# Kernel optimization log

Hardware: AMD Instinct MI355X
Metric: run time of the kernel (lower is better)

## Reference

```python
import jax, jax.numpy as jnp
import numpy as np

NUM_EMBEDDINGS = 1024
EMBEDDING_DIM = 256
BETA = 0.25


def setup_inputs() -> dict:
    key = jax.random.key(0)
    kz, ke = jax.random.split(key)
    z = jax.random.normal(kz, (32, EMBEDDING_DIM, 32, 32), dtype=jnp.float32)
    # codebook initialized uniform(-1/K, 1/K) as in the torch module
    emb = jax.random.uniform(ke, (NUM_EMBEDDINGS, EMBEDDING_DIM), dtype=jnp.float32,
                             minval=-1.0 / NUM_EMBEDDINGS, maxval=1.0 / NUM_EMBEDDINGS)
    return {"z": z, "emb": emb}


def reference(z, emb):
    B, C, H, W = z.shape
    # [B, C, H, W] -> [B*H*W, C]
    z_flat = jnp.transpose(z, (0, 2, 3, 1)).reshape(-1, C)
    # squared L2 distances to every codebook entry: [N, K]
    distances = (jnp.sum(z_flat ** 2, axis=1, keepdims=True)
                 + jnp.sum(emb ** 2, axis=1)
                 - 2.0 * jnp.matmul(z_flat, emb.T))
    indices = jnp.argmin(distances, axis=1).reshape(B, H, W)  # int32 [B, H, W]
    # gather codebook vectors, back to [B, C, H, W]
    z_q = jnp.transpose(emb[indices], (0, 3, 1, 2))
    sg = jax.lax.stop_gradient
    loss = (BETA * jnp.mean((sg(z_q) - z) ** 2)
            + jnp.mean((z_q - sg(z)) ** 2))
    # straight-through estimator
    z_q_st = z + sg(z_q - z)
    return z_q_st, indices, loss
```

## Files before the change

### kernel.cpp

```cpp
#include <hip/hip_runtime.h>

#define CDIM 256
#define HW 1024
#define NROWS 32768
#define KCODES 1024
#define ZQ_ELEMS 8388608
#define IDX_OFF ZQ_ELEMS
#define LOSS_OFF (ZQ_ELEMS + NROWS)
#define FLT_BIG 3.402823466e+38f
#define ZT_OFF 5513232ull

typedef _Float16 f16;
typedef _Float16 f16x8 __attribute__((ext_vector_type(8)));
typedef float f32x4 __attribute__((ext_vector_type(4)));
typedef float f32x16 __attribute__((ext_vector_type(16)));

__device__ __forceinline__ void glds16(const void* g, void* l) {
    __builtin_amdgcn_global_load_lds(
        (const __attribute__((address_space(1))) unsigned int*)g,
        (__attribute__((address_space(3))) unsigned int*)l,
        16, 0, 0);
}

__device__ __forceinline__ unsigned int pack_f16x2(f16 a, f16 b) {
    unsigned short ua = *(unsigned short*)&a, ub = *(unsigned short*)&b;
    return (unsigned int)ua | ((unsigned int)ub << 16);
}

__device__ __forceinline__ float np_sumsq_256(const float* __restrict__ a) {
    float half[2];
#pragma unroll
    for (int h = 0; h < 2; ++h) {
        const float* p = a + h * 128;
        float r[8];
#pragma unroll
        for (int j = 0; j < 8; ++j) r[j] = __fmul_rn(p[j], p[j]);
#pragma unroll
        for (int i = 8; i < 128; i += 8) {
#pragma unroll
            for (int j = 0; j < 8; ++j)
                r[j] = __fadd_rn(r[j], __fmul_rn(p[i + j], p[i + j]));
        }
        float ta = __fadd_rn(__fadd_rn(r[0], r[1]), __fadd_rn(r[2], r[3]));
        float tb = __fadd_rn(__fadd_rn(r[4], r[5]), __fadd_rn(r[6], r[7]));
        half[h] = __fadd_rn(ta, tb);
    }
    return __fadd_rn(half[0], half[1]);
}

__device__ __forceinline__ bool lex_lt(float s1, int k1, float s2, int k2) {
    return (s1 < s2) || (s1 == s2 && k1 < k2);
}

__device__ __forceinline__ void top2_merge(float& a1, int& ka1, float& a2, int& ka2,
                                           float b1, int kb1, float b2, int kb2) {
    if (lex_lt(b1, kb1, a1, ka1)) {
        float t1 = a1; int tk1 = ka1;
        a1 = b1; ka1 = kb1;
        if (lex_lt(b2, kb2, t1, tk1)) { a2 = b2; ka2 = kb2; }
        else                          { a2 = t1; ka2 = tk1; }
    } else {
        if (lex_lt(b1, kb1, a2, ka2)) { a2 = b1; ka2 = kb1; }
    }
}

__global__ void __launch_bounds__(256)
prep_kernel(const float* __restrict__ z, const float* __restrict__ emb,
            f16* __restrict__ A, float* __restrict__ z2,
            float* __restrict__ e2, f16* __restrict__ e16,
            float* __restrict__ z_t) {
    const int t = threadIdx.x;
    if (blockIdx.x >= 1024) {
        const int gid = (blockIdx.x - 1024) * 256 + t;
        const int k = gid >> 5, seg = gid & 31;
        const float* src = emb + (size_t)k * CDIM + seg * 8;
        float4 v0 = *(const float4*)src;
        float4 v1 = *(const float4*)(src + 4);
        float s[8] = { v0.x, v0.y, v0.z, v0.w, v1.x, v1.y, v1.z, v1.w };
        f16 h[8], l[8];
#pragma unroll
        for (int j = 0; j < 8; ++j) {
            float sv = s[j] * 1024.0f;
            h[j] = (f16)sv;
            float r = __fsub_rn(sv, (float)h[j]);
            l[j] = (f16)r;
        }
        uint4 hv, lv;
        hv.x = pack_f16x2(h[0], h[1]); hv.y = pack_f16x2(h[2], h[3]);
        hv.z = pack_f16x2(h[4], h[5]); hv.w = pack_f16x2(h[6], h[7]);
        lv.x = pack_f16x2(l[0], l[1]); lv.y = pack_f16x2(l[2], l[3]);
        lv.z = pack_f16x2(l[4], l[5]); lv.w = pack_f16x2(l[6], l[7]);
        *(uint4*)(e16 + (size_t)k * 512 + seg * 8) = hv;
        *(uint4*)(e16 + (size_t)k * 512 + 256 + seg * 8) = lv;
        if (seg == 0) e2[k] = np_sumsq_256(emb + (size_t)k * CDIM);
        return;
    }
    __shared__ __align__(16) float z_lds[32 * 260];
    const int n0 = blockIdx.x * 32;
    const int b = n0 >> 10, hw0 = n0 & 1023;
    const float* zbase = z + (size_t)b * (CDIM * HW) + hw0;
#pragma unroll
    for (int p = 0; p < 8; ++p) {
        int id = p * 256 + t;
        int c = id >> 3;
        int m4 = id & 7;
        float4 v = *(const float4*)(zbase + (size_t)c * HW + m4 * 4);
        z_lds[(m4 * 4 + 0) * 260 + c] = v.x;
        z_lds[(m4 * 4 + 1) * 260 + c] = v.y;
        z_lds[(m4 * 4 + 2) * 260 + c] = v.z;
        z_lds[(m4 * 4 + 3) * 260 + c] = v.w;
    }
    __syncthreads();
    if (t < 32) z2[n0 + t] = np_sumsq_256(&z_lds[t * 260]);

    if (z_t) {
#pragma unroll
        for (int p = 0; p < 8; ++p) {
            int id = p * 256 + t;
            int m = id >> 6;
            int c4 = (id & 63) * 4;
            float4 v = { z_lds[m * 260 + c4],     z_lds[m * 260 + c4 + 1],
                         z_lds[m * 260 + c4 + 2], z_lds[m * 260 + c4 + 3] };
            *(float4*)&z_t[(size_t)(n0 + m) * CDIM + c4] = v;
        }
    }

    const int lane = t & 63, wave = t >> 6;
    const int half = lane >> 5;
    const int seg = lane & 31;
#pragma unroll
    for (int rr = 0; rr < 8; ++rr) {
        const int m = wave * 8 + rr;
        const float* zr = &z_lds[m * 260 + seg * 8];
        f16 o[8];
#pragma unroll
        for (int j = 0; j < 8; ++j) {
            float sv = zr[j] * 16.0f;
            f16 hh = (f16)sv;
            if (half) {
                float r = __fsub_rn(sv, (float)hh);
                o[j] = (f16)r;
            } else {
                o[j] = hh;
            }
        }
        uint4 ov;
        ov.x = pack_f16x2(o[0], o[1]); ov.y = pack_f16x2(o[2], o[3]);
        ov.z = pack_f16x2(o[4], o[5]); ov.w = pack_f16x2(o[6], o[7]);
        *(uint4*)(A + (size_t)(n0 + m) * 512 + half * 256 + seg * 8) = ov;
    }
}

__global__ void __launch_bounds__(256, 3)
gemm_argmin_kernel(const f16* __restrict__ A, const f16* __restrict__ B,
                   const float* __restrict__ z2, const float* __restrict__ e2,
                   float4* __restrict__ tile_red) {
    __shared__ __align__(16) f16 c1_lds[2][128 * 32];
    __shared__ __align__(16) f16 c2_lds[2][128 * 32];
    __shared__ __align__(16) f16 z_lds[2][128 * 32];
    __shared__ __align__(16) float4 red_lds[2 * 128];
    __shared__ float e2_lds[128];

    const int t = threadIdx.x;
    const int lane = t & 63, wave = t >> 6;
    const int Ntile = blockIdx.x & 255;
    const int Mtile = blockIdx.x >> 8;
    const int wc = (wave & 1) * 64;
    const int wz = (wave >> 1) * 64;
    const int c31 = lane & 31, hhalf = lane >> 5;
    const int gsw = (c31 >> 1) & 3;

    if (t < 128) e2_lds[t] = e2[Mtile * 128 + t];

    const int s0 = 2 * wave, s1 = s0 + 1;
    const char* Cbase = (const char*)(B + (size_t)Mtile * 128 * 512);
    const char* Zbase = (const char*)(A + (size_t)Ntile * 128 * 512);
    const int lrow = lane >> 2;
    const int lsw = ((lane & 3) ^ ((lrow >> 1) & 3)) * 16;
    const char* cg0 = Cbase + (size_t)(s0 * 16 + lrow) * 1024 + lsw;
    const char* cg1 = Cbase + (size_t)(s1 * 16 + lrow) * 1024 + lsw;
    const char* zg0 = Zbase + (size_t)(s0 * 16 + lrow) * 1024 + lsw;
    const char* zg1 = Zbase + (size_t)(s1 * 16 + lrow) * 1024 + lsw;

    int crow32[2], zrow32[2], g8[2];
#pragma unroll
    for (int i = 0; i < 2; ++i) crow32[i] = (wc + i * 32 + c31) * 32;
#pragma unroll
    for (int j = 0; j < 2; ++j) zrow32[j] = (wz + j * 32 + c31) * 32;
#pragma unroll
    for (int ks = 0; ks < 2; ++ks) g8[ks] = ((2 * ks + hhalf) ^ gsw) * 8;

    f32x16 acc[2][2] = {};

    glds16(cg0,       &c1_lds[0][s0 * 512]);
    glds16(cg1,       &c1_lds[0][s1 * 512]);
    glds16(cg0 + 512, &c2_lds[0][s0 * 512]);
    glds16(cg1 + 512, &c2_lds[0][s1 * 512]);
    glds16(zg0,       &z_lds[0][s0 * 512]);
    glds16(zg1,       &z_lds[0][s1 * 512]);
    __syncthreads();

    for (int kk = 0; kk < 16; ++kk) {
        const int buf = kk & 1;
        if (kk < 15) {
            const int nb = buf ^ 1;
            const int ko = (kk + 1) * 64;
            const int ko2 = (ko + 512) & 1023;
            glds16(cg0 + ko,  &c1_lds[nb][s0 * 512]);
            glds16(cg1 + ko,  &c1_lds[nb][s1 * 512]);
            glds16(cg0 + ko2, &c2_lds[nb][s0 * 512]);
            glds16(cg1 + ko2, &c2_lds[nb][s1 * 512]);
            glds16(zg0 + ko,  &z_lds[nb][s0 * 512]);
            glds16(zg1 + ko,  &z_lds[nb][s1 * 512]);
        }

#pragma unroll
        for (int ks = 0; ks < 2; ++ks) {
            f16x8 zf[2], cf1[2], cf2[2];
#pragma unroll
            for (int j = 0; j < 2; ++j)
                zf[j] = *(const f16x8*)&z_lds[buf][zrow32[j] + g8[ks]];
#pragma unroll
            for (int i = 0; i < 2; ++i) {
                cf1[i] = *(const f16x8*)&c1_lds[buf][crow32[i] + g8[ks]];
                cf2[i] = *(const f16x8*)&c2_lds[buf][crow32[i] + g8[ks]];
            }
#pragma unroll
            for (int i = 0; i < 2; ++i)
#pragma unroll
                for (int j = 0; j < 2; ++j) {
                    acc[i][j] = __builtin_amdgcn_mfma_f32_32x32x16_f16(cf1[i], zf[j], acc[i][j], 0, 0, 0);
                    acc[i][j] = __builtin_amdgcn_mfma_f32_32x32x16_f16(cf2[i], zf[j], acc[i][j], 0, 0, 0);
                }
        }
        __syncthreads();
    }

#pragma unroll
    for (int j = 0; j < 2; ++j) {
        const float z2v = z2[Ntile * 128 + wz + j * 32 + c31];
        float s1 = FLT_BIG, s2 = FLT_BIG;
        int k1 = KCODES, k2 = KCODES;
#pragma unroll
        for (int i = 0; i < 2; ++i) {
            const int cbase = wc + i * 32 + 4 * hhalf;
#pragma unroll
            for (int r = 0; r < 16; ++r) {
                const int clocal = cbase + (r & 3) + 8 * (r >> 2);
                const float e2r = e2_lds[clocal];
                const float d = __fsub_rn(__fadd_rn(z2v, e2r),
                                          __fmul_rn(acc[i][j][r], 1.220703125e-4f));
                const int kc = Mtile * 128 + clocal;
                if (lex_lt(d, kc, s1, k1)) { s2 = s1; k2 = k1; s1 = d; k1 = kc; }
                else if (lex_lt(d, kc, s2, k2)) { s2 = d; k2 = kc; }
            }
        }
        float b1 = __shfl_xor(s1, 32); int kb1 = __shfl_xor(k1, 32);
        float b2 = __shfl_xor(s2, 32); int kb2 = __shfl_xor(k2, 32);
        top2_merge(s1, k1, s2, k2, b1, kb1, b2, kb2);
        if (hhalf == 0) {
            float4 st;
            st.x = s1; st.y = __int_as_float(k1);
            st.z = s2; st.w = __int_as_float(k2);
            red_lds[(wave & 1) * 128 + wz + j * 32 + c31] = st;
        }
    }
    __syncthreads();
    if (t < 128) {
        float4 a = red_lds[t];
        float4 b = red_lds[128 + t];
        float a1 = a.x, a2 = a.z; int ka1 = __float_as_int(a.y), ka2 = __float_as_int(a.w);
        top2_merge(a1, ka1, a2, ka2, b.x, __float_as_int(b.y), b.z, __float_as_int(b.w));
        float4 o;
        o.x = a1; o.y = __int_as_float(ka1); o.z = a2; o.w = __int_as_float(ka2);
        tile_red[(size_t)(Ntile * 128 + t) * 8 + Mtile] = o;
    }
}

__global__ void __launch_bounds__(256)
rescore_kernel(const float* __restrict__ z, const float* __restrict__ emb,
               const float* __restrict__ z2, const float* __restrict__ e2,
               const float4* __restrict__ tile_red, const float* __restrict__ z_t,
               float* __restrict__ out_idx_f, int* __restrict__ ws_idx) {
    const int gid = blockIdx.x * 256 + threadIdx.x;
    const int n = gid >> 2, q = gid & 3;

    float s[4]; int k[4];
    const float4 v0 = tile_red[(size_t)n * 8 + q * 2];
    const float4 v1 = tile_red[(size_t)n * 8 + q * 2 + 1];
    s[0] = v0.x; k[0] = __float_as_int(v0.y);
    s[1] = v0.z; k[1] = __float_as_int(v0.w);
    s[2] = v1.x; k[2] = __float_as_int(v1.y);
    s[3] = v1.z; k[3] = __float_as_int(v1.w);

    float s1 = FLT_BIG; int k1 = KCODES;
#pragma unroll
    for (int i = 0; i < 4; ++i)
        if (lex_lt(s[i], k[i], s1, k1)) { s1 = s[i]; k1 = k[i]; }
#pragma unroll
    for (int m = 1; m <= 2; m <<= 1) {
        float bs = __shfl_xor(s1, m); int bk2 = __shfl_xor(k1, m);
        if (lex_lt(bs, bk2, s1, k1)) { s1 = bs; k1 = bk2; }
    }
    const float thr = s1 + 1.0e-4f;
    int cnt = 0;
#pragma unroll
    for (int i = 0; i < 4; ++i) cnt += (s[i] <= thr) ? 1 : 0;
    cnt += __shfl_xor(cnt, 1);
    cnt += __shfl_xor(cnt, 2);

    int bk = k1;
    if (cnt > 1) {
        int kk[4];
#pragma unroll
        for (int i = 0; i < 4; ++i) kk[i] = (s[i] <= thr) ? k[i] : k1;
        float accs[4] = { 0.f, 0.f, 0.f, 0.f };
        if (z_t) {
            const float* zr = z_t + (size_t)n * CDIM;
            for (int c0 = 0; c0 < 256; c0 += 4) {
                const float4 zv = *(const float4*)&zr[c0];
#pragma unroll
                for (int j = 0; j < 4; ++j) {
                    float4 ev = *(const float4*)&emb[(size_t)kk[j] * CDIM + c0];
                    accs[j] = fmaf(zv.x, ev.x, accs[j]);
                    accs[j] = fmaf(zv.y, ev.y, accs[j]);
                    accs[j] = fmaf(zv.z, ev.z, accs[j]);
                    accs[j] = fmaf(zv.w, ev.w, accs[j]);
                }
            }
        } else {
            const float* zb = z + (size_t)(n >> 10) * (CDIM * HW) + (n & 1023);
            for (int c0 = 0; c0 < 256; c0 += 4) {
                float zc0 = zb[(size_t)(c0 + 0) * HW];
                float zc1 = zb[(size_t)(c0 + 1) * HW];
                float zc2 = zb[(size_t)(c0 + 2) * HW];
                float zc3 = zb[(size_t)(c0 + 3) * HW];
#pragma unroll
                for (int j = 0; j < 4; ++j) {
                    float4 ev = *(const float4*)&emb[(size_t)kk[j] * CDIM + c0];
                    accs[j] = fmaf(zc0, ev.x, accs[j]);
                    accs[j] = fmaf(zc1, ev.y, accs[j]);
                    accs[j] = fmaf(zc2, ev.z, accs[j]);
                    accs[j] = fmaf(zc3, ev.w, accs[j]);
                }
            }
        }
        float bd = FLT_BIG; bk = KCODES;
        const float z2n = z2[n];
#pragma unroll
        for (int j = 0; j < 4; ++j) {
            float d = __fsub_rn(__fadd_rn(z2n, e2[kk[j]]), accs[j] + accs[j]);
            if (lex_lt(d, kk[j], bd, bk)) { bd = d; bk = kk[j]; }
        }
#pragma unroll
        for (int m = 1; m <= 2; m <<= 1) {
            float bs = __shfl_xor(bd, m); int bb = __shfl_xor(bk, m);
            if (lex_lt(bs, bb, bd, bk)) { bd = bs; bk = bb; }
        }
    }
    if (q == 0) {
        out_idx_f[n] = (float)bk;
        ws_idx[n] = bk;
    }
}

__global__ void __launch_bounds__(256)
gather_kernel(const float* __restrict__ z, const float* __restrict__ emb,
              const int* __restrict__ ws_idx, float* __restrict__ out_zq,
              float* __restrict__ partials) {
    const int t = threadIdx.x;
    const int b = blockIdx.x >> 5;
    const int cg = blockIdx.x & 31;
    const int hw4 = t * 4;

    const int4 iv = *(const int4*)&ws_idx[b * HW + hw4];
    const float* zb = z + (size_t)b * (CDIM * HW) + hw4;
    float* ob = out_zq + (size_t)b * (CDIM * HW) + hw4;
    const float* e0p = emb + (size_t)iv.x * CDIM;
    const float* e1p = emb + (size_t)iv.y * CDIM;
    const float* e2p = emb + (size_t)iv.z * CDIM;
    const float* e3p = emb + (size_t)iv.w * CDIM;

    float lsum = 0.f;
#pragma unroll
    for (int c = cg * 8; c < cg * 8 + 8; ++c) {
        float4 zv = *(const float4*)&zb[(size_t)c * HW];
        float d0 = e0p[c] - zv.x;
        float d1 = e1p[c] - zv.y;
        float d2 = e2p[c] - zv.z;
        float d3 = e3p[c] - zv.w;
        float4 ov = { zv.x + d0, zv.y + d1, zv.z + d2, zv.w + d3 };
        *(float4*)&ob[(size_t)c * HW] = ov;
        lsum = fmaf(d0, d0, lsum);
        lsum = fmaf(d1, d1, lsum);
        lsum = fmaf(d2, d2, lsum);
        lsum = fmaf(d3, d3, lsum);
    }
#pragma unroll
    for (int off = 32; off > 0; off >>= 1) lsum += __shfl_down(lsum, off);
    __shared__ float wsum[4];
    if ((t & 63) == 0) wsum[t >> 6] = lsum;
    __syncthreads();
    if (t == 0) partials[blockIdx.x] = (wsum[0] + wsum[1]) + (wsum[2] + wsum[3]);
}

__global__ void loss_kernel(const float* __restrict__ partials, float* __restrict__ out_loss) {
    const int t = threadIdx.x;
    float4 v4 = *(const float4*)&partials[t * 4];
    float v = (v4.x + v4.y) + (v4.z + v4.w);
#pragma unroll
    for (int off = 32; off > 0; off >>= 1) v += __shfl_down(v, off);
    __shared__ float wsum[4];
    if ((t & 63) == 0) wsum[t >> 6] = v;
    __syncthreads();
    if (t == 0) {
        float total = (wsum[0] + wsum[1]) + (wsum[2] + wsum[3]);
        out_loss[0] = 1.25f * total / 8388608.0f;
    }
}

extern "C" void kernel_launch(void* const* d_in, const int* in_sizes, int n_in,
                              void* d_out, int out_size, void* d_ws, size_t ws_size,
                              hipStream_t stream) {
    const float* z   = (const float*)d_in[0];
    const float* emb = (const float*)d_in[1];
    float* out = (float*)d_out;

    f16* A = (f16*)d_out;

    char* w = (char*)d_ws;
    float*  e2       = (float*)(w + 0);
    float*  z2       = (float*)(w + 4096);
    f16*    e16      = (f16*)(w + 135168);
    float4* tile_red = (float4*)(w + 1183744);
    int*    ws_idx   = (int*)(w + 5378048);
    float*  partials = (float*)(w + 5509120);

    const size_t zt_need = ZT_OFF + (size_t)NROWS * CDIM * sizeof(float);
    float* z_t = (ws_size >= zt_need) ? (float*)(w + ZT_OFF) : nullptr;

    hipLaunchKernelGGL(prep_kernel, dim3(1152), dim3(256), 0, stream,
                       z, emb, A, z2, e2, e16, z_t);
    hipLaunchKernelGGL(gemm_argmin_kernel, dim3(2048), dim3(256), 0, stream,
                       A, e16, z2, e2, tile_red);
    hipLaunchKernelGGL(rescore_kernel, dim3(512), dim3(256), 0, stream,
                       z, emb, z2, e2, tile_red, z_t, out + IDX_OFF, ws_idx);
    hipLaunchKernelGGL(gather_kernel, dim3(1024), dim3(256), 0, stream,
                       z, emb, ws_idx, out, partials);
    hipLaunchKernelGGL(loss_kernel, dim3(1), dim3(256), 0, stream,
                       partials, out + LOSS_OFF);
}
```

Before: 226.5 us.

## Enlarge GEMM-argmin block tile to 256 rows with 8 waves

The distance GEMM block now covers 256 z rows by 128 codes using 512 threads (8 waves), halving the grid. Each code tile loaded into LDS is reused across twice as many rows, which cuts redundant codebook loads and LDS staging per output. Launch bounds are raised to (512,4), which asks the compiler for 8 waves per SIMD and so caps registers hard; the 64-float accumulators per thread may spill. The larger LDS footprint (over 72KB per block) also limits how many blocks fit on a CU.

```diff
diff --git a/kernel.cpp b/kernel.cpp
--- a/kernel.cpp
+++ b/kernel.cpp
@@ -151,20 +151,20 @@
     }
 }
 
-__global__ void __launch_bounds__(256, 3)
+__global__ void __launch_bounds__(512, 4)
 gemm_argmin_kernel(const f16* __restrict__ A, const f16* __restrict__ B,
                    const float* __restrict__ z2, const float* __restrict__ e2,
                    float4* __restrict__ tile_red) {
     __shared__ __align__(16) f16 c1_lds[2][128 * 32];
     __shared__ __align__(16) f16 c2_lds[2][128 * 32];
-    __shared__ __align__(16) f16 z_lds[2][128 * 32];
-    __shared__ __align__(16) float4 red_lds[2 * 128];
+    __shared__ __align__(16) f16 z_lds[2][256 * 32];
+    __shared__ __align__(16) float4 red_lds[2 * 256];
     __shared__ float e2_lds[128];
 
     const int t = threadIdx.x;
     const int lane = t & 63, wave = t >> 6;
-    const int Ntile = blockIdx.x & 255;
-    const int Mtile = blockIdx.x >> 8;
+    const int Ntile = blockIdx.x & 127;
+    const int Mtile = blockIdx.x >> 7;
     const int wc = (wave & 1) * 64;
     const int wz = (wave >> 1) * 64;
     const int c31 = lane & 31, hhalf = lane >> 5;
@@ -172,15 +172,16 @@
 
     if (t < 128) e2_lds[t] = e2[Mtile * 128 + t];
 
-    const int s0 = 2 * wave, s1 = s0 + 1;
     const char* Cbase = (const char*)(B + (size_t)Mtile * 128 * 512);
-    const char* Zbase = (const char*)(A + (size_t)Ntile * 128 * 512);
+    const char* Zbase = (const char*)(A + (size_t)Ntile * 256 * 512);
     const int lrow = lane >> 2;
     const int lsw = ((lane & 3) ^ ((lrow >> 1) & 3)) * 16;
-    const char* cg0 = Cbase + (size_t)(s0 * 16 + lrow) * 1024 + lsw;
-    const char* cg1 = Cbase + (size_t)(s1 * 16 + lrow) * 1024 + lsw;
-    const char* zg0 = Zbase + (size_t)(s0 * 16 + lrow) * 1024 + lsw;
-    const char* zg1 = Zbase + (size_t)(s1 * 16 + lrow) * 1024 + lsw;
+    const char* cg  = Cbase + (size_t)(wave * 16 + lrow) * 1024 + lsw;
+    const char* zg0 = Zbase + (size_t)((2 * wave) * 16 + lrow) * 1024 + lsw;
+    const char* zg1 = Zbase + (size_t)((2 * wave + 1) * 16 + lrow) * 1024 + lsw;
+    const int woffc  = wave * 512;
+    const int woffz0 = (2 * wave) * 512;
+    const int woffz1 = (2 * wave + 1) * 512;
 
     int crow32[2], zrow32[2], g8[2];
 #pragma unroll
@@ -192,12 +193,10 @@
 
     f32x16 acc[2][2] = {};
 
-    glds16(cg0,       &c1_lds[0][s0 * 512]);
-    glds16(cg1,       &c1_lds[0][s1 * 512]);
-    glds16(cg0 + 512, &c2_lds[0][s0 * 512]);
-    glds16(cg1 + 512, &c2_lds[0][s1 * 512]);
-    glds16(zg0,       &z_lds[0][s0 * 512]);
-    glds16(zg1,       &z_lds[0][s1 * 512]);
+    glds16(cg,        &c1_lds[0][woffc]);
+    glds16(cg + 512,  &c2_lds[0][woffc]);
+    glds16(zg0,       &z_lds[0][woffz0]);
+    glds16(zg1,       &z_lds[0][woffz1]);
     __syncthreads();
 
     for (int kk = 0; kk < 16; ++kk) {
@@ -206,12 +205,10 @@
             const int nb = buf ^ 1;
             const int ko = (kk + 1) * 64;
             const int ko2 = (ko + 512) & 1023;
-            glds16(cg0 + ko,  &c1_lds[nb][s0 * 512]);
-            glds16(cg1 + ko,  &c1_lds[nb][s1 * 512]);
-            glds16(cg0 + ko2, &c2_lds[nb][s0 * 512]);
-            glds16(cg1 + ko2, &c2_lds[nb][s1 * 512]);
-            glds16(zg0 + ko,  &z_lds[nb][s0 * 512]);
-            glds16(zg1 + ko,  &z_lds[nb][s1 * 512]);
+            glds16(cg + ko,   &c1_lds[nb][woffc]);
+            glds16(cg + ko2,  &c2_lds[nb][woffc]);
+            glds16(zg0 + ko,  &z_lds[nb][woffz0]);
+            glds16(zg1 + ko,  &z_lds[nb][woffz1]);
         }
 
 #pragma unroll
@@ -238,7 +235,7 @@
 
 #pragma unroll
     for (int j = 0; j < 2; ++j) {
-        const float z2v = z2[Ntile * 128 + wz + j * 32 + c31];
+        const float z2v = z2[Ntile * 256 + wz + j * 32 + c31];
         float s1 = FLT_BIG, s2 = FLT_BIG;
         int k1 = KCODES, k2 = KCODES;
 #pragma unroll
@@ -262,18 +259,18 @@
             float4 st;
             st.x = s1; st.y = __int_as_float(k1);
             st.z = s2; st.w = __int_as_float(k2);
-            red_lds[(wave & 1) * 128 + wz + j * 32 + c31] = st;
+            red_lds[(wave & 1) * 256 + wz + j * 32 + c31] = st;
         }
     }
     __syncthreads();
-    if (t < 128) {
+    if (t < 256) {
         float4 a = red_lds[t];
-        float4 b = red_lds[128 + t];
+        float4 b = red_lds[256 + t];
         float a1 = a.x, a2 = a.z; int ka1 = __float_as_int(a.y), ka2 = __float_as_int(a.w);
         top2_merge(a1, ka1, a2, ka2, b.x, __float_as_int(b.y), b.z, __float_as_int(b.w));
         float4 o;
         o.x = a1; o.y = __int_as_float(ka1); o.z = a2; o.w = __int_as_float(ka2);
-        tile_red[(size_t)(Ntile * 128 + t) * 8 + Mtile] = o;
+        tile_red[(size_t)(Ntile * 256 + t) * 8 + Mtile] = o;
     }
 }
 
@@ -441,7 +438,7 @@
 
     hipLaunchKernelGGL(prep_kernel, dim3(1152), dim3(256), 0, stream,
                        z, emb, A, z2, e2, e16, z_t);
-    hipLaunchKernelGGL(gemm_argmin_kernel, dim3(2048), dim3(256), 0, stream,
+    hipLaunchKernelGGL(gemm_argmin_kernel, dim3(1024), dim3(512), 0, stream,
                        A, e16, z2, e2, tile_red);
     hipLaunchKernelGGL(rescore_kernel, dim3(512), dim3(256), 0, stream,
                        z, emb, z2, e2, tile_red, z_t, out + IDX_OFF, ws_idx);
```

Result: slower. 270.5 us (+19.4%).
